# Performance work log

Hardware: AMD Instinct MI355X
Metric: run time of the kernel (lower is better)

## Reference

```python
import jax, jax.numpy as jnp
import numpy as np

TEMPERATURE = 0.5
EPS = 1e-12  # matches torch F.normalize eps


def _l2_normalize(x):
    norm = jnp.linalg.norm(x, axis=-1, keepdims=True)
    return x / jnp.maximum(norm, EPS)


def setup_inputs() -> dict:
    key = jax.random.key(0)
    k1, k2, k3 = jax.random.split(key, 3)
    N, D = 16384, 128
    self_predictions = jax.random.normal(k1, (N, D), dtype=jnp.float32)
    pos_predictions = jax.random.normal(k2, (N, D), dtype=jnp.float32)
    labels1 = jax.random.randint(k3, (N,), 0, 100, dtype=jnp.int64)
    return {
        "self_predictions": self_predictions,
        "pos_predictions": pos_predictions,
        "labels1": labels1,
    }


def reference(self_predictions, pos_predictions, labels1):
    N = labels1.shape[0]
    a = _l2_normalize(self_predictions)  # [N, D]
    b = _l2_normalize(pos_predictions)   # [N, D]
    # cosine similarity of already-normalized rows == dot product (GEMM form)
    sim = jnp.einsum("nd,md->nm", a, b)  # [N, N]
    neg_mask = (labels1[:, None] != labels1[None, :]).astype(sim.dtype)  # 1 - mask
    neg = jnp.exp(-sim / TEMPERATURE) * neg_mask
    return neg.sum() / (N * (N - 1))
```

## Files before the change

### kernel.cpp

```cpp
#include <hip/hip_runtime.h>

typedef unsigned char u8;
typedef unsigned short u16;
typedef float f32x4 __attribute__((ext_vector_type(4)));
typedef long l2 __attribute__((ext_vector_type(2)));

#define NROWS 16384
#define DIM 128

#define NEG2LOG2E -2.8853900817779268f

__global__ __launch_bounds__(256) void norm_kernel(
    const float* __restrict__ a, const float* __restrict__ b,
    u8* __restrict__ aO, u8* __restrict__ bO)
{
    int tid  = threadIdx.x;
    int lane = tid & 63;
    int w    = tid >> 6;
    long row = (long)blockIdx.x * 4 + w;

    const float2 va = ((const float2*)(a + row * DIM))[lane];
    float sa = va.x * va.x + va.y * va.y;
    #pragma unroll
    for (int off = 32; off; off >>= 1) sa += __shfl_xor(sa, off, 64);
    float inva = 1.0f / fmaxf(sqrtf(sa), 1e-12f);
    unsigned int pa = (unsigned int)__builtin_amdgcn_cvt_pk_fp8_f32(
        va.x * inva, va.y * inva, 0, false);
    ((u16*)(aO + row * DIM))[lane] = (u16)(pa & 0xffffu);

    const float2 vb = ((const float2*)(b + row * DIM))[lane];
    float sb = vb.x * vb.x + vb.y * vb.y;
    #pragma unroll
    for (int off = 32; off; off >>= 1) sb += __shfl_xor(sb, off, 64);
    float invb = NEG2LOG2E / fmaxf(sqrtf(sb), 1e-12f);
    unsigned int pb = (unsigned int)__builtin_amdgcn_cvt_pk_fp8_f32(
        vb.x * invb, vb.y * invb, 0, false);
    ((u16*)(bO + row * DIM))[lane] = (u16)(pb & 0xffffu);
}

__global__ __launch_bounds__(256, 3) void gemm_kernel(
    const u8* __restrict__ A, const u8* __restrict__ B,
    const int* __restrict__ labels, float* __restrict__ partials)
{
    __shared__ u8 sA[16384];
    __shared__ u8 sB[2][16384];

    int tid  = threadIdx.x;
    int lane = tid & 63;
    int w    = tid >> 6;
    int wr   = w >> 1;
    int wc   = w & 1;
    int mrow = lane & 15;
    int q    = lane >> 4;

    int rowBase = blockIdx.y * 128;
    int colBase = blockIdx.x * 512;

    int m0 = tid >> 3;
    int p0 = tid & 7;
    int srcOff = m0 * 128 + ((p0 ^ (m0 & 7)) << 4);
    int ldsOff = (tid - lane) * 16;

    const u8* gA = A + (size_t)rowBase * DIM + srcOff;
    const u8* gB = B + (size_t)colBase * DIM + srcOff;

    {
        const u8* gpA = gA;
        const u8* gpB = gB;
        u8* lpA = &sA[ldsOff];
        u8* lpB = &sB[0][ldsOff];
        #pragma unroll
        for (int it = 0; it < 4; it++) {
            __builtin_amdgcn_global_load_lds(
                (const __attribute__((address_space(1))) void*)gpA,
                (__attribute__((address_space(3))) void*)lpA, 16, 0, 0);
            __builtin_amdgcn_global_load_lds(
                (const __attribute__((address_space(1))) void*)gpB,
                (__attribute__((address_space(3))) void*)lpB, 16, 0, 0);
            gpA += 4096; gpB += 4096; lpA += 4096; lpB += 4096;
        }
    }

    int iBase = rowBase + wr * 64 + q * 4;
    int li[16];
    #pragma unroll
    for (int mi = 0; mi < 4; mi++)
        #pragma unroll
        for (int r = 0; r < 4; r++)
            li[mi * 4 + r] = labels[iBase + mi * 16 + r];

    int aOff[4], bOff[4];
    #pragma unroll
    for (int mi = 0; mi < 4; mi++) {
        int m = wr * 64 + mi * 16 + mrow;
        aOff[mi] = m * 128 + (((q << 1) ^ (m & 7)) << 4);
        int n = wc * 64 + mi * 16 + mrow;
        bOff[mi] = n * 128 + (((q << 1) ^ (n & 7)) << 4);
    }

    __syncthreads();

    l2 aF[2][4];
    #pragma unroll
    for (int h = 0; h < 2; h++)
        #pragma unroll
        for (int mi = 0; mi < 4; mi++)
            aF[h][mi] = *(const l2*)(sA + (aOff[mi] ^ (h << 4)));

    float s = 0.0f;

    #pragma unroll
    for (int jt = 0; jt < 4; jt++) {
        if (jt < 3) {
            const u8* gp = gB + (jt + 1) * (128 * DIM);
            u8* lp = &sB[(jt + 1) & 1][ldsOff];
            #pragma unroll
            for (int it = 0; it < 4; it++) {
                __builtin_amdgcn_global_load_lds(
                    (const __attribute__((address_space(1))) void*)gp,
                    (__attribute__((address_space(3))) void*)lp, 16, 0, 0);
                gp += 4096; lp += 4096;
            }
        }

        int jBase = colBase + jt * 128 + wc * 64 + mrow;
        int lj[4];
        #pragma unroll
        for (int ni = 0; ni < 4; ni++)
            lj[ni] = labels[jBase + ni * 16];

        const u8* sb = sB[jt & 1];
        f32x4 acc[4][4];
        #pragma unroll
        for (int mi = 0; mi < 4; mi++)
            #pragma unroll
            for (int ni = 0; ni < 4; ni++)
                acc[mi][ni] = (f32x4){0.f, 0.f, 0.f, 0.f};

        #pragma unroll
        for (int h = 0; h < 2; h++) {
            l2 bF[4];
            #pragma unroll
            for (int ni = 0; ni < 4; ni++)
                bF[ni] = *(const l2*)(sb + (bOff[ni] ^ (h << 4)));
            #pragma unroll
            for (int mi = 0; mi < 4; mi++)
                #pragma unroll
                for (int ni = 0; ni < 4; ni++) {
                    acc[mi][ni] = __builtin_amdgcn_mfma_f32_16x16x32_fp8_fp8(
                        aF[h][mi][0], bF[ni][0], acc[mi][ni], 0, 0, 0);
                    acc[mi][ni] = __builtin_amdgcn_mfma_f32_16x16x32_fp8_fp8(
                        aF[h][mi][1], bF[ni][1], acc[mi][ni], 0, 0, 0);
                }
        }

        float s0 = 0.0f, s1 = 0.0f;
        #pragma unroll
        for (int mi = 0; mi < 4; mi++)
            #pragma unroll
            for (int ni = 0; ni < 4; ni++)
                #pragma unroll
                for (int r = 0; r < 4; r++) {
                    float e = __builtin_amdgcn_exp2f(acc[mi][ni][r]);
                    float m = (li[mi * 4 + r] != lj[ni]) ? e : 0.0f;
                    if (r & 1) s1 += m; else s0 += m;
                }
        s += s0 + s1;

        __syncthreads();
    }

    #pragma unroll
    for (int off = 32; off; off >>= 1) s += __shfl_xor(s, off, 64);

    float* red = (float*)sA;
    if (lane == 0) red[w] = s;
    __syncthreads();
    if (tid == 0) {
        constexpr float SCALE = (float)(1.0 / (16384.0 * 16383.0));
        float t = (red[0] + red[1]) + (red[2] + red[3]);
        partials[blockIdx.y * 32 + blockIdx.x] = t * SCALE;
    }
}

__global__ __launch_bounds__(256) void reduce_kernel(
    const float* __restrict__ partials, float* __restrict__ out)
{
    int tid = threadIdx.x;
    const float4* p4 = (const float4*)partials;
    float s = 0.0f;
    #pragma unroll 4
    for (int i = tid; i < 1024; i += 256) {
        float4 v = p4[i];
        s += (v.x + v.y) + (v.z + v.w);
    }
    #pragma unroll
    for (int off = 32; off; off >>= 1) s += __shfl_xor(s, off, 64);
    __shared__ float red[4];
    if ((tid & 63) == 0) red[tid >> 6] = s;
    __syncthreads();
    if (tid == 0) out[0] = (red[0] + red[1]) + (red[2] + red[3]);
}

extern "C" void kernel_launch(void* const* d_in, const int* in_sizes, int n_in,
                              void* d_out, int out_size, void* d_ws, size_t ws_size,
                              hipStream_t stream) {
    const float* self_p = (const float*)d_in[0];
    const float* pos_p  = (const float*)d_in[1];
    const int*   labels = (const int*)d_in[2];
    float* out = (float*)d_out;

    u8* aB = (u8*)d_ws;
    u8* bB = aB + (size_t)NROWS * DIM;
    float* partials = (float*)(bB + (size_t)NROWS * DIM);

    norm_kernel<<<NROWS / 4, 256, 0, stream>>>(self_p, pos_p, aB, bB);
    gemm_kernel<<<dim3(32, 128), 256, 0, stream>>>(aB, bB, labels, partials);
    reduce_kernel<<<1, 256, 0, stream>>>(partials, out);
}
```

Before: 129.2 us.

## Drop label masking from GEMM via per-label correction and use scaled K=128 MFMA

The main GEMM now sums exp over all pairs with no label comparison, and no longer loads labels. A new bucket kernel groups rows by label. A correction kernel then computes the same-label block sums per label and subtracts them in the final reduction. The inner product also switches from pairs of 16x16x32 fp8 MFMAs to a single 16x16x128 scaled f8f6f4 MFMA with unit scales. This adds two small extra launches and a single-block bucketing pass. The correction assumes at most 320 rows per label and exactly 100 labels.

```diff
diff --git a/kernel.cpp b/kernel.cpp
--- a/kernel.cpp
+++ b/kernel.cpp
@@ -4,11 +4,16 @@
 typedef unsigned short u16;
 typedef float f32x4 __attribute__((ext_vector_type(4)));
 typedef long l2 __attribute__((ext_vector_type(2)));
+typedef int i32x4 __attribute__((ext_vector_type(4)));
+typedef int i32x8 __attribute__((ext_vector_type(8)));
 
 #define NROWS 16384
 #define DIM 128
 
 #define NEG2LOG2E -2.8853900817779268f
+#define SCALE ((float)(1.0 / (16384.0 * 16383.0)))
+
+#define SCALE1 0x7F7F7F7F
 
 __global__ __launch_bounds__(256) void norm_kernel(
     const float* __restrict__ a, const float* __restrict__ b,
@@ -38,9 +43,32 @@
     ((u16*)(bO + row * DIM))[lane] = (u16)(pb & 0xffffu);
 }
 
+__global__ __launch_bounds__(256) void bucket_kernel(
+    const int* __restrict__ labels, int* __restrict__ offs, int* __restrict__ idx)
+{
+    __shared__ int cnt[100];
+    __shared__ int cur[100];
+    int tid = threadIdx.x;
+    if (tid < 100) cnt[tid] = 0;
+    __syncthreads();
+    for (int i = tid; i < NROWS; i += 256)
+        atomicAdd(&cnt[labels[i]], 1);
+    __syncthreads();
+    if (tid == 0) {
+        int run = 0;
+        for (int l = 0; l < 100; l++) { cur[l] = run; offs[l] = run; run += cnt[l]; }
+        offs[100] = run;
+    }
+    __syncthreads();
+    for (int i = tid; i < NROWS; i += 256) {
+        int p = atomicAdd(&cur[labels[i]], 1);
+        idx[p] = i;
+    }
+}
+
 __global__ __launch_bounds__(256, 3) void gemm_kernel(
     const u8* __restrict__ A, const u8* __restrict__ B,
-    const int* __restrict__ labels, float* __restrict__ partials)
+    float* __restrict__ partials)
 {
     __shared__ u8 sA[16384];
     __shared__ u8 sB[2][16384];
@@ -81,14 +109,6 @@
         }
     }
 
-    int iBase = rowBase + wr * 64 + q * 4;
-    int li[16];
-    #pragma unroll
-    for (int mi = 0; mi < 4; mi++)
-        #pragma unroll
-        for (int r = 0; r < 4; r++)
-            li[mi * 4 + r] = labels[iBase + mi * 16 + r];
-
     int aOff[4], bOff[4];
     #pragma unroll
     for (int mi = 0; mi < 4; mi++) {
@@ -100,12 +120,12 @@
 
     __syncthreads();
 
-    l2 aF[2][4];
-    #pragma unroll
-    for (int h = 0; h < 2; h++)
-        #pragma unroll
-        for (int mi = 0; mi < 4; mi++)
-            aF[h][mi] = *(const l2*)(sA + (aOff[mi] ^ (h << 4)));
+    i32x8 a8[4];
+    #pragma unroll
+    for (int mi = 0; mi < 4; mi++) {
+        *((i32x4*)&a8[mi])     = *(const i32x4*)(sA + aOff[mi]);
+        *((i32x4*)&a8[mi] + 1) = *(const i32x4*)(sA + (aOff[mi] ^ 16));
+    }
 
     float s = 0.0f;
 
@@ -123,13 +143,14 @@
             }
         }
 
-        int jBase = colBase + jt * 128 + wc * 64 + mrow;
-        int lj[4];
-        #pragma unroll
-        for (int ni = 0; ni < 4; ni++)
-            lj[ni] = labels[jBase + ni * 16];
-
         const u8* sb = sB[jt & 1];
+        i32x8 b8[4];
+        #pragma unroll
+        for (int ni = 0; ni < 4; ni++) {
+            *((i32x4*)&b8[ni])     = *(const i32x4*)(sb + bOff[ni]);
+            *((i32x4*)&b8[ni] + 1) = *(const i32x4*)(sb + (bOff[ni] ^ 16));
+        }
+
         f32x4 acc[4][4];
         #pragma unroll
         for (int mi = 0; mi < 4; mi++)
@@ -138,21 +159,11 @@
                 acc[mi][ni] = (f32x4){0.f, 0.f, 0.f, 0.f};
 
         #pragma unroll
-        for (int h = 0; h < 2; h++) {
-            l2 bF[4];
+        for (int mi = 0; mi < 4; mi++)
             #pragma unroll
             for (int ni = 0; ni < 4; ni++)
-                bF[ni] = *(const l2*)(sb + (bOff[ni] ^ (h << 4)));
-            #pragma unroll
-            for (int mi = 0; mi < 4; mi++)
-                #pragma unroll
-                for (int ni = 0; ni < 4; ni++) {
-                    acc[mi][ni] = __builtin_amdgcn_mfma_f32_16x16x32_fp8_fp8(
-                        aF[h][mi][0], bF[ni][0], acc[mi][ni], 0, 0, 0);
-                    acc[mi][ni] = __builtin_amdgcn_mfma_f32_16x16x32_fp8_fp8(
-                        aF[h][mi][1], bF[ni][1], acc[mi][ni], 0, 0, 0);
-                }
-        }
+                acc[mi][ni] = __builtin_amdgcn_mfma_scale_f32_16x16x128_f8f6f4(
+                    a8[mi], b8[ni], acc[mi][ni], 0, 0, 0, SCALE1, 0, SCALE1);
 
         float s0 = 0.0f, s1 = 0.0f;
         #pragma unroll
@@ -162,8 +173,7 @@
                 #pragma unroll
                 for (int r = 0; r < 4; r++) {
                     float e = __builtin_amdgcn_exp2f(acc[mi][ni][r]);
-                    float m = (li[mi * 4 + r] != lj[ni]) ? e : 0.0f;
-                    if (r & 1) s1 += m; else s0 += m;
+                    if (r & 1) s1 += e; else s0 += e;
                 }
         s += s0 + s1;
 
@@ -177,23 +187,87 @@
     if (lane == 0) red[w] = s;
     __syncthreads();
     if (tid == 0) {
-        constexpr float SCALE = (float)(1.0 / (16384.0 * 16383.0));
         float t = (red[0] + red[1]) + (red[2] + red[3]);
         partials[blockIdx.y * 32 + blockIdx.x] = t * SCALE;
     }
 }
 
+#define KMAX 320
+#define RSTR 144
+__global__ __launch_bounds__(512) void corr_kernel(
+    const u8* __restrict__ A, const u8* __restrict__ B,
+    const int* __restrict__ offs, const int* __restrict__ idx,
+    float* __restrict__ corrP)
+{
+    __shared__ u8 sA[KMAX * RSTR];
+    __shared__ u8 sB[KMAX * RSTR];
+    __shared__ float red[8];
+
+    int l   = blockIdx.x;
+    int o0  = offs[l];
+    int k   = offs[l + 1] - o0;
+    if (k > KMAX) k = KMAX;
+    int tid = threadIdx.x;
+
+    for (int t = tid; t < k * 8; t += 512) {
+        int r = t >> 3, g = t & 7;
+        int row = idx[o0 + r];
+        *(float4*)(sA + r * RSTR + g * 16) = *(const float4*)(A + (size_t)row * DIM + g * 16);
+        *(float4*)(sB + r * RSTR + g * 16) = *(const float4*)(B + (size_t)row * DIM + g * 16);
+    }
+    __syncthreads();
+
+    int lane = tid & 63, w = tid >> 6;
+    int mrow = lane & 15, q = lane >> 4;
+    int nt = (k + 15) >> 4;
+    float s = 0.0f;
+
+    for (int tp = w; tp < nt * nt; tp += 8) {
+        int ti = tp / nt, tj = tp - ti * nt;
+        const u8* pa = sA + (ti * 16 + mrow) * RSTR + q * 32;
+        const u8* pb = sB + (tj * 16 + mrow) * RSTR + q * 32;
+        i32x8 aF, bF;
+        *((i32x4*)&aF)     = *(const i32x4*)pa;
+        *((i32x4*)&aF + 1) = *(const i32x4*)(pa + 16);
+        *((i32x4*)&bF)     = *(const i32x4*)pb;
+        *((i32x4*)&bF + 1) = *(const i32x4*)(pb + 16);
+        f32x4 acc = (f32x4){0.f, 0.f, 0.f, 0.f};
+        acc = __builtin_amdgcn_mfma_scale_f32_16x16x128_f8f6f4(
+            aF, bF, acc, 0, 0, 0, SCALE1, 0, SCALE1);
+        int i0 = ti * 16 + q * 4;
+        int j  = tj * 16 + mrow;
+        #pragma unroll
+        for (int r = 0; r < 4; r++) {
+            float e = __builtin_amdgcn_exp2f(acc[r]);
+            s += ((i0 + r) < k && j < k) ? e : 0.0f;
+        }
+    }
+
+    #pragma unroll
+    for (int off = 32; off; off >>= 1) s += __shfl_xor(s, off, 64);
+    if (lane == 0) red[w] = s;
+    __syncthreads();
+    if (tid == 0) {
+        float t = 0.f;
+        #pragma unroll
+        for (int i = 0; i < 8; i++) t += red[i];
+        corrP[l] = t * SCALE;
+    }
+}
+
 __global__ __launch_bounds__(256) void reduce_kernel(
-    const float* __restrict__ partials, float* __restrict__ out)
+    const float* __restrict__ gP, const float* __restrict__ cP,
+    float* __restrict__ out)
 {
     int tid = threadIdx.x;
-    const float4* p4 = (const float4*)partials;
+    const float4* p4 = (const float4*)gP;
     float s = 0.0f;
     #pragma unroll 4
     for (int i = tid; i < 1024; i += 256) {
         float4 v = p4[i];
         s += (v.x + v.y) + (v.z + v.w);
     }
+    if (tid < 100) s -= cP[tid];
     #pragma unroll
     for (int off = 32; off; off >>= 1) s += __shfl_xor(s, off, 64);
     __shared__ float red[4];
@@ -212,9 +286,14 @@
 
     u8* aB = (u8*)d_ws;
     u8* bB = aB + (size_t)NROWS * DIM;
-    float* partials = (float*)(bB + (size_t)NROWS * DIM);
-
+    float* gemmP = (float*)(bB + (size_t)NROWS * DIM);
+    float* corrP = gemmP + 4096;
+    int*   offs  = (int*)(corrP + 128);
+    int*   idx   = offs + 128;
+
+    bucket_kernel<<<1, 256, 0, stream>>>(labels, offs, idx);
     norm_kernel<<<NROWS / 4, 256, 0, stream>>>(self_p, pos_p, aB, bB);
-    gemm_kernel<<<dim3(32, 128), 256, 0, stream>>>(aB, bB, labels, partials);
-    reduce_kernel<<<1, 256, 0, stream>>>(partials, out);
-}
+    gemm_kernel<<<dim3(32, 128), 256, 0, stream>>>(aB, bB, gemmP);
+    corr_kernel<<<100, 512, 0, stream>>>(aB, bB, offs, idx, corrP);
+    reduce_kernel<<<1, 256, 0, stream>>>(gemmP, corrP, out);
+}
```

After: 150.7 us. 1.17x slower.

## Use scaled 16x16x128 FP8 MFMA and widen norm kernel loads

Applied to the files above, without the earlier changes.

Replaces pairs of 16x16x32 FP8 MFMAs with a single MFMA-scale 16x16x128 f8f6f4 instruction per tile, passing unity exponent scales, and loads the fragments as 32-byte vectors from LDS. This reduces the instruction count and issue overhead of the GEMM inner loop. The norm kernel now handles two rows per wavefront with float4 loads and packed 4-byte FP8 stores, which halves its grid. The fragment layout for the K=128 instruction has to match the swizzled LDS layout, and getting it wrong would reorder the K dimension.

```diff
diff --git a/kernel.cpp b/kernel.cpp
--- a/kernel.cpp
+++ b/kernel.cpp
@@ -3,12 +3,16 @@
 typedef unsigned char u8;
 typedef unsigned short u16;
 typedef float f32x4 __attribute__((ext_vector_type(4)));
-typedef long l2 __attribute__((ext_vector_type(2)));
+typedef int i32x4 __attribute__((ext_vector_type(4)));
+typedef int i32x8 __attribute__((ext_vector_type(8)));
 
 #define NROWS 16384
 #define DIM 128
 
 #define NEG2LOG2E -2.8853900817779268f
+#define SCALE ((float)(1.0 / (16384.0 * 16383.0)))
+
+#define SCALE1 0x7F7F7F7F
 
 __global__ __launch_bounds__(256) void norm_kernel(
     const float* __restrict__ a, const float* __restrict__ b,
@@ -17,25 +21,27 @@
     int tid  = threadIdx.x;
     int lane = tid & 63;
     int w    = tid >> 6;
-    long row = (long)blockIdx.x * 4 + w;
-
-    const float2 va = ((const float2*)(a + row * DIM))[lane];
-    float sa = va.x * va.x + va.y * va.y;
-    #pragma unroll
-    for (int off = 32; off; off >>= 1) sa += __shfl_xor(sa, off, 64);
+    int half = lane >> 5;
+    int l32  = lane & 31;
+    long row = (long)blockIdx.x * 8 + w * 2 + half;
+
+    const float4 va = ((const float4*)(a + row * DIM))[l32];
+    float sa = va.x * va.x + va.y * va.y + va.z * va.z + va.w * va.w;
+    #pragma unroll
+    for (int off = 16; off; off >>= 1) sa += __shfl_xor(sa, off, 64);
     float inva = 1.0f / fmaxf(sqrtf(sa), 1e-12f);
-    unsigned int pa = (unsigned int)__builtin_amdgcn_cvt_pk_fp8_f32(
-        va.x * inva, va.y * inva, 0, false);
-    ((u16*)(aO + row * DIM))[lane] = (u16)(pa & 0xffffu);
-
-    const float2 vb = ((const float2*)(b + row * DIM))[lane];
-    float sb = vb.x * vb.x + vb.y * vb.y;
-    #pragma unroll
-    for (int off = 32; off; off >>= 1) sb += __shfl_xor(sb, off, 64);
+    int pa = __builtin_amdgcn_cvt_pk_fp8_f32(va.x * inva, va.y * inva, 0, false);
+    pa = __builtin_amdgcn_cvt_pk_fp8_f32(va.z * inva, va.w * inva, pa, true);
+    ((int*)(aO + row * DIM))[l32] = pa;
+
+    const float4 vb = ((const float4*)(b + row * DIM))[l32];
+    float sb = vb.x * vb.x + vb.y * vb.y + vb.z * vb.z + vb.w * vb.w;
+    #pragma unroll
+    for (int off = 16; off; off >>= 1) sb += __shfl_xor(sb, off, 64);
     float invb = NEG2LOG2E / fmaxf(sqrtf(sb), 1e-12f);
-    unsigned int pb = (unsigned int)__builtin_amdgcn_cvt_pk_fp8_f32(
-        vb.x * invb, vb.y * invb, 0, false);
-    ((u16*)(bO + row * DIM))[lane] = (u16)(pb & 0xffffu);
+    int pb = __builtin_amdgcn_cvt_pk_fp8_f32(vb.x * invb, vb.y * invb, 0, false);
+    pb = __builtin_amdgcn_cvt_pk_fp8_f32(vb.z * invb, vb.w * invb, pb, true);
+    ((int*)(bO + row * DIM))[l32] = pb;
 }
 
 __global__ __launch_bounds__(256, 3) void gemm_kernel(
@@ -100,12 +106,12 @@
 
     __syncthreads();
 
-    l2 aF[2][4];
-    #pragma unroll
-    for (int h = 0; h < 2; h++)
-        #pragma unroll
-        for (int mi = 0; mi < 4; mi++)
-            aF[h][mi] = *(const l2*)(sA + (aOff[mi] ^ (h << 4)));
+    i32x8 a8[4];
+    #pragma unroll
+    for (int mi = 0; mi < 4; mi++) {
+        *((i32x4*)&a8[mi])     = *(const i32x4*)(sA + aOff[mi]);
+        *((i32x4*)&a8[mi] + 1) = *(const i32x4*)(sA + (aOff[mi] ^ 16));
+    }
 
     float s = 0.0f;
 
@@ -130,6 +136,13 @@
             lj[ni] = labels[jBase + ni * 16];
 
         const u8* sb = sB[jt & 1];
+        i32x8 b8[4];
+        #pragma unroll
+        for (int ni = 0; ni < 4; ni++) {
+            *((i32x4*)&b8[ni])     = *(const i32x4*)(sb + bOff[ni]);
+            *((i32x4*)&b8[ni] + 1) = *(const i32x4*)(sb + (bOff[ni] ^ 16));
+        }
+
         f32x4 acc[4][4];
         #pragma unroll
         for (int mi = 0; mi < 4; mi++)
@@ -138,21 +151,11 @@
                 acc[mi][ni] = (f32x4){0.f, 0.f, 0.f, 0.f};
 
         #pragma unroll
-        for (int h = 0; h < 2; h++) {
-            l2 bF[4];
+        for (int mi = 0; mi < 4; mi++)
             #pragma unroll
             for (int ni = 0; ni < 4; ni++)
-                bF[ni] = *(const l2*)(sb + (bOff[ni] ^ (h << 4)));
-            #pragma unroll
-            for (int mi = 0; mi < 4; mi++)
-                #pragma unroll
-                for (int ni = 0; ni < 4; ni++) {
-                    acc[mi][ni] = __builtin_amdgcn_mfma_f32_16x16x32_fp8_fp8(
-                        aF[h][mi][0], bF[ni][0], acc[mi][ni], 0, 0, 0);
-                    acc[mi][ni] = __builtin_amdgcn_mfma_f32_16x16x32_fp8_fp8(
-                        aF[h][mi][1], bF[ni][1], acc[mi][ni], 0, 0, 0);
-                }
-        }
+                acc[mi][ni] = __builtin_amdgcn_mfma_scale_f32_16x16x128_f8f6f4(
+                    a8[mi], b8[ni], acc[mi][ni], 0, 0, 0, SCALE1, 0, SCALE1);
 
         float s0 = 0.0f, s1 = 0.0f;
         #pragma unroll
@@ -177,17 +180,16 @@
     if (lane == 0) red[w] = s;
     __syncthreads();
     if (tid == 0) {
-        constexpr float SCALE = (float)(1.0 / (16384.0 * 16383.0));
         float t = (red[0] + red[1]) + (red[2] + red[3]);
         partials[blockIdx.y * 32 + blockIdx.x] = t * SCALE;
     }
 }
 
 __global__ __launch_bounds__(256) void reduce_kernel(
-    const float* __restrict__ partials, float* __restrict__ out)
+    const float* __restrict__ gP, float* __restrict__ out)
 {
     int tid = threadIdx.x;
-    const float4* p4 = (const float4*)partials;
+    const float4* p4 = (const float4*)gP;
     float s = 0.0f;
     #pragma unroll 4
     for (int i = tid; i < 1024; i += 256) {
@@ -212,9 +214,9 @@
 
     u8* aB = (u8*)d_ws;
     u8* bB = aB + (size_t)NROWS * DIM;
-    float* partials = (float*)(bB + (size_t)NROWS * DIM);
-
-    norm_kernel<<<NROWS / 4, 256, 0, stream>>>(self_p, pos_p, aB, bB);
-    gemm_kernel<<<dim3(32, 128), 256, 0, stream>>>(aB, bB, labels, partials);
-    reduce_kernel<<<1, 256, 0, stream>>>(partials, out);
-}
+    float* gemmP = (float*)(bB + (size_t)NROWS * DIM);
+
+    norm_kernel<<<NROWS / 8, 256, 0, stream>>>(self_p, pos_p, aB, bB);
+    gemm_kernel<<<dim3(32, 128), 256, 0, stream>>>(aB, bB, labels, gemmP);
+    reduce_kernel<<<1, 256, 0, stream>>>(gemmP, out);
+}
```

After: 118.6 us. 1.09x faster.
